# Optimization experiments

Hardware: AMD Instinct MI355X
Metric: run time of the kernel (lower is better)

## Reference

```python
import jax, jax.numpy as jnp
import numpy as np

B, NB, NS, C, HID, NP, NH = 8, 2048, 1024, 768, 3072, 1024, 6
HD = C // NH


def _ln(x, w, b):
    mu = x.mean(-1, keepdims=True)
    var = ((x - mu) ** 2).mean(-1, keepdims=True)
    return (x - mu) / jnp.sqrt(var + 1e-5) * w + b


def _gelu(z):
    return jax.nn.gelu(z, approximate=False)  # torch nn.GELU default = exact erf


def setup_inputs() -> dict:
    key = jax.random.key(0)
    ks = jax.random.split(key, 16)
    p = lambda i, shape: (jax.random.normal(ks[i], shape, jnp.float32) * 0.02)
    inp = {
        'x_b': jax.random.normal(ks[0], (B, NB, C), jnp.float32),
        'x_s': jax.random.normal(ks[1], (B, NS, C), jnp.float32),
        # token_types[0,0]=0 -> KV is computed (no stale cache), as on the first call
        'token_types': jax.random.randint(ks[2], (B, NS), 0, 2, jnp.int32).at[0, 0].set(0),
        'base_idxs': jax.random.randint(ks[3], (B, NP), -3, NB).astype(jnp.int32),
        'ln1_w': jnp.ones(C, jnp.float32), 'ln1_b': jnp.zeros(C, jnp.float32),
        'ln2_w': jnp.ones(C, jnp.float32), 'ln2_b': jnp.zeros(C, jnp.float32),
        'ln3_w': jnp.ones(C, jnp.float32), 'ln3_b': jnp.zeros(C, jnp.float32),
        'Wq': p(4, (C, C)), 'Wkv': p(5, (C, 2 * C)),
        'es_w1': p(6, (C, HID)), 'es_b1': jnp.zeros(HID, jnp.float32),
        'es_w2': p(7, (HID, C)), 'es_b2': jnp.zeros(C, jnp.float32),
        'el_w1': p(8, (C, HID)), 'el_b1': jnp.zeros(HID, jnp.float32),
        'el_w2': p(9, (HID, C)), 'el_b2': jnp.zeros(C, jnp.float32),
        'mlp_w1': p(10, (C, 4 * C)), 'mlp_b1': jnp.zeros(4 * C, jnp.float32),
        'mlp_w2': p(11, (4 * C, C)), 'mlp_b2': jnp.zeros(C, jnp.float32),
    }
    return inp


def reference(x_b, x_s, token_types, base_idxs,
              ln1_w, ln1_b, ln2_w, ln2_b, ln3_w, ln3_b,
              Wq, Wkv, es_w1, es_b1, es_w2, es_b2,
              el_w1, el_b1, el_w2, el_b2,
              mlp_w1, mlp_b1, mlp_w2, mlp_b2):
    Bn, Ns, Cd = x_s.shape
    # --- norm1/norm2 + cross-attention (q from x_s, kv from x_b) ---
    xs_n = _ln(x_s, ln1_w, ln1_b)
    xb_n = _ln(x_b, ln2_w, ln2_b)
    q = (xs_n @ Wq).reshape(Bn, Ns, NH, HD).transpose(0, 2, 1, 3)          # (B,H,Ns,hd)
    kv = (xb_n @ Wkv).reshape(Bn, -1, 2, NH, HD).transpose(2, 0, 3, 1, 4)  # (2,B,H,Nb,hd)
    k_, v_ = kv[0], kv[1]
    attn = jax.nn.softmax(jnp.einsum('bhqd,bhkd->bhqk', q, k_) * (HD ** -0.5), axis=-1)
    ctx = jnp.einsum('bhqk,bhkd->bhqd', attn, v_).transpose(0, 2, 1, 3).reshape(Bn, Ns, Cd)
    # --- 2-expert MoE MLP routed by token_types (0 -> expert_s, 1 -> expert_l) ---
    out_s = _gelu(ctx @ es_w1 + es_b1) @ es_w2 + es_b2
    out_l = _gelu(ctx @ el_w1 + el_b1) @ el_w2 + el_b2
    tt = token_types[..., None]
    moe = jnp.where(tt == 0, out_s, 0.0) + jnp.where(tt == 1, out_l, 0.0)
    x = x_s + moe
    # --- residual MLP ---
    x = x + (_gelu(_ln(x, ln3_w, ln3_b) @ mlp_w1 + mlp_b1) @ mlp_w2 + mlp_b2)
    x_norm = x / jnp.maximum(jnp.linalg.norm(x, axis=-1, keepdims=True), 1e-12)
    # --- masked-token kernel (vectorized over batch, masking replaces gather) ---
    nh = base_idxs.shape[1] // 2
    ids = base_idxs[:, :nh]
    mask = ids >= 0                                        # (B,nh)
    idc = jnp.where(mask, ids, 0)
    tokens = jnp.take_along_axis(x_b, idc[:, :, None], axis=1) * mask[..., None]
    sc = jnp.einsum('bic,bjc->bij', tokens, tokens) / jnp.sqrt(jnp.float32(Cd))
    kbias = jnp.where(mask, 0.0, -1e9)[:, None, :]
    aw = jax.nn.softmax(sc + kbias, axis=-1)
    agg = jnp.einsum('bij,bjc->bic', aw, tokens)
    cnt = mask.sum(-1)
    ksum = (agg * mask[..., None]).sum(1) / jnp.maximum(cnt, 1)[:, None]
    kn = ksum / jnp.maximum(jnp.linalg.norm(ksum, axis=-1, keepdims=True), 1e-12)
    has = (cnt > 0)[:, None]
    kernel = jnp.where(has, kn, 0.0)                        # (B,C)
    pos = jnp.where(has, (jnp.einsum('bnc,bc->bn', x_norm, kernel) + 1.0) / 2.0, 0.0)
    # --- top-k selection with data-dependent valid_k and straight-through binarize ---
    kk = Ns // 8
    topv, topi = jax.lax.top_k(pos, kk)
    cnt65 = (pos > 0.65).sum(-1)
    vk = jnp.minimum(kk, jnp.maximum(kk - 10, cnt65))
    keep = jnp.arange(kk)[None, :] < vk[:, None]
    vals = topv * keep
    sel = vals[:, :, None] * jax.nn.one_hot(topi, Ns, dtype=x.dtype)
    binary = (sel > 0.0).astype(x.dtype)
    sel = sel + jax.lax.stop_gradient(binary - sel)
    return sel, topi, pos, x, kernel[:, None, :]
```

## Files before the change

### kernel.cpp

```cpp
#include <hip/hip_runtime.h>
#include <hip/hip_bf16.h>
#include <math.h>

#define B_   8
#define NB_  2048
#define NS_  1024
#define Cc_  768
#define HID_ 3072
#define NP_  1024
#define NH_  6
#define HD_  128

__device__ __forceinline__ float gelu_exact(float v) {
  return 0.5f * v * (1.0f + erff(v * 0.7071067811865476f));
}

__device__ __forceinline__ void split3(float v, unsigned short& h,
                                       unsigned short& m, unsigned short& l) {
  unsigned hb = __float_as_uint(v) & 0xffff0000u;
  float r1 = v - __uint_as_float(hb);
  unsigned mb = __float_as_uint(r1) & 0xffff0000u;
  float r2 = r1 - __uint_as_float(mb);
  unsigned lb = __float_as_uint(r2) & 0xffff0000u;
  h = (unsigned short)(hb >> 16);
  m = (unsigned short)(mb >> 16);
  l = (unsigned short)(lb >> 16);
}

typedef short bf16x8 __attribute__((ext_vector_type(8)));
typedef float f32x4 __attribute__((ext_vector_type(4)));

#define BLOCK_REDUCE_ADD(red, tid)                                              \
  for (int off_ = 128; off_; off_ >>= 1) {                                      \
    if ((tid) < off_) red[(tid)] += red[(tid) + off_];                          \
    __syncthreads();                                                            \
  }

__global__ __launch_bounds__(256) void ln_split(
    const float* __restrict__ x, unsigned short* __restrict__ y,
    const float* __restrict__ w, const float* __restrict__ b) {
  __shared__ float red[256];
  int row = blockIdx.x, tid = threadIdx.x;
  const float* xr = x + (size_t)row * Cc_;
  float v0 = xr[tid], v1 = xr[tid + 256], v2 = xr[tid + 512];
  red[tid] = v0 + v1 + v2;
  __syncthreads();
  BLOCK_REDUCE_ADD(red, tid);
  float mu = red[0] / (float)Cc_;
  __syncthreads();
  float d0 = v0 - mu, d1 = v1 - mu, d2 = v2 - mu;
  red[tid] = d0 * d0 + d1 * d1 + d2 * d2;
  __syncthreads();
  BLOCK_REDUCE_ADD(red, tid);
  float var = red[0] / (float)Cc_;
  float rs = 1.0f / sqrtf(var + 1e-5f);
  unsigned short* yr = y + (size_t)row * 2304;
  float vals[3] = {d0 * rs * w[tid] + b[tid],
                   d1 * rs * w[tid + 256] + b[tid + 256],
                   d2 * rs * w[tid + 512] + b[tid + 512]};
#pragma unroll
  for (int t = 0; t < 3; ++t) {
    int c = tid + (t << 8);
    unsigned short h16, m16, l16;
    split3(vals[t], h16, m16, l16);
    yr[c] = h16; yr[768 + c] = m16; yr[1536 + c] = l16;
  }
}

__global__ __launch_bounds__(256) void split_kernel(
    const float* __restrict__ x, unsigned short* __restrict__ y) {
  size_t idx = (size_t)blockIdx.x * 256 + threadIdx.x;
  int c = (int)(idx % Cc_);
  int row = (int)(idx / Cc_);
  unsigned short h16, m16, l16;
  split3(x[idx], h16, m16, l16);
  unsigned short* yr = y + (size_t)row * 2304;
  yr[c] = h16; yr[768 + c] = m16; yr[1536 + c] = l16;
}

__global__ __launch_bounds__(256) void qsplit(
    const float* __restrict__ q, unsigned short* __restrict__ qp) {
  int idx = blockIdx.x * 256 + threadIdx.x;
  int c = idx & 127, m = (idx >> 7) & 1023, h = idx >> 17;
  float v = q[(size_t)m * 768 + h * 128 + c];
  unsigned short h16, m16, l16;
  split3(v, h16, m16, l16);
  size_t base = (size_t)h * 393216 + (size_t)m * 384;
  qp[base + c] = h16; qp[base + 128 + c] = m16; qp[base + 256 + c] = l16;
}

__global__ __launch_bounds__(256) void ksplit(
    const float* __restrict__ kv, unsigned short* __restrict__ kp) {
  int idx = blockIdx.x * 256 + threadIdx.x;
  int c = idx & 127, n = (idx >> 7) & 2047, h = idx >> 18;
  float v = kv[(size_t)n * 1536 + h * 128 + c];
  unsigned short h16, m16, l16;
  split3(v, h16, m16, l16);
  size_t base = (size_t)h * 786432 + (size_t)n * 384;
  kp[base + c] = h16; kp[base + 128 + c] = m16; kp[base + 256 + c] = l16;
}

__global__ __launch_bounds__(256) void rownorm_kernel(
    const float* __restrict__ x, float* __restrict__ y) {
  __shared__ float red[256];
  int row = blockIdx.x, tid = threadIdx.x;
  const float* xr = x + (size_t)row * Cc_;
  float* yr = y + (size_t)row * Cc_;
  float v0 = xr[tid], v1 = xr[tid + 256], v2 = xr[tid + 512];
  red[tid] = v0 * v0 + v1 * v1 + v2 * v2;
  __syncthreads();
  BLOCK_REDUCE_ADD(red, tid);
  float den = fmaxf(sqrtf(red[0]), 1e-12f);
  yr[tid]       = v0 / den;
  yr[tid + 256] = v1 / den;
  yr[tid + 512] = v2 / den;
}

__global__ __launch_bounds__(256) void wconv(
    const float* __restrict__ W, unsigned short* __restrict__ out,
    int K, int N, int ldw, int ncol0) {
  int k = blockIdx.x * 256 + threadIdx.x;
  int n = blockIdx.y;
  float v = W[(size_t)k * ldw + ncol0 + n];
  unsigned short h16, m16, l16;
  split3(v, h16, m16, l16);
  size_t base = (size_t)n * 3 * K;
  out[base + k] = h16;
  out[base + K + k] = m16;
  out[base + 2 * K + k] = l16;
}

template <int EPI, bool AGATHER, bool MDEV>
__global__ __launch_bounds__(256) void mgemm(
    const unsigned short* __restrict__ Ap, const unsigned short* __restrict__ Bp,
    float* __restrict__ Cf, unsigned short* __restrict__ Cs,
    const float* __restrict__ bias,
    const int* __restrict__ perm, const int* __restrict__ mdev,
    int M, int N, int K, int ldc, int Kout, int nsplit,
    long azs, long bzs, long zstride, float scale) {
  __shared__ unsigned short As[2][8192];
  __shared__ unsigned short Bs[2][8192];
  int z = blockIdx.z;
  int gx = gridDim.x;
  int id = blockIdx.y * gx + blockIdx.x;
  int per = (gx * gridDim.y) >> 3;
  int nid = (id & 7) * per + (id >> 3);
  int bx = nid % gx, by = nid / gx;
  int Me = MDEV ? mdev[0] : M;
  int m0 = by * 128, n0 = bx * 128;
  if (MDEV && m0 >= Me) return;
  const unsigned short* ApB = Ap + (size_t)z * azs;
  const unsigned short* BpB = Bp + (size_t)z * bzs;
  int tid = threadIdx.x;
  int lane = tid & 63, w = tid >> 6;
  int wr = w >> 1, wc = w & 1;
  int K3 = 3 * K;
  int tps = K >> 6;
  int KT = 6 * tps;
  int span = KT / nsplit;
  int zr = z % nsplit;
  int tt0 = zr * span, tt1 = tt0 + span;

  const unsigned short* agp[4];
  const unsigned short* bgp[4];
  int wswz[4];
#pragma unroll
  for (int p = 0; p < 4; ++p) {
    int r = (tid >> 3) + 32 * p;
    int ma = m0 + r;
    if (MDEV) ma = min(ma, Me - 1);
    if (AGATHER) ma = perm[ma];
    agp[p] = ApB + (size_t)ma * K3 + (tid & 7) * 8;
    bgp[p] = BpB + (size_t)(n0 + r) * K3 + (tid & 7) * 8;
    wswz[p] = r * 64 + (((tid & 7) ^ (r & 7)) << 3);
  }

  f32x4 acc[4][4];
  f32x4 zero4 = {0.f, 0.f, 0.f, 0.f};
#pragma unroll
  for (int i = 0; i < 4; ++i)
#pragma unroll
    for (int j = 0; j < 4; ++j) acc[i][j] = zero4;

  int kg = lane >> 4;
  int frm[4], frn[4];
#pragma unroll
  for (int f = 0; f < 4; ++f) {
    frm[f] = wr * 64 + f * 16 + (lane & 15);
    frn[f] = wc * 64 + f * 16 + (lane & 15);
  }

  bf16x8 ra[4], rb[4];
  {
    int seg = tt0 / tps, kt = tt0 - seg * tps;
    int pa = (0x210100u >> (4 * seg)) & 0xF;
    int pb = (0x012010u >> (4 * seg)) & 0xF;
    size_t ao = (size_t)(pa * K + kt * 64);
    size_t bo = (size_t)(pb * K + kt * 64);
#pragma unroll
    for (int p = 0; p < 4; ++p) {
      ra[p] = *(const bf16x8*)(agp[p] + ao);
      rb[p] = *(const bf16x8*)(bgp[p] + bo);
    }
  }

  for (int tt = tt0; tt < tt1; ++tt) {
    int cur = tt & 1;
#pragma unroll
    for (int p = 0; p < 4; ++p) {
      *(bf16x8*)&As[cur][wswz[p]] = ra[p];
      *(bf16x8*)&Bs[cur][wswz[p]] = rb[p];
    }
    if (tt + 1 < tt1) {
      int seg = (tt + 1) / tps, kt = (tt + 1) - seg * tps;
      int pa = (0x210100u >> (4 * seg)) & 0xF;
      int pb = (0x012010u >> (4 * seg)) & 0xF;
      size_t ao = (size_t)(pa * K + kt * 64);
      size_t bo = (size_t)(pb * K + kt * 64);
#pragma unroll
      for (int p = 0; p < 4; ++p) {
        ra[p] = *(const bf16x8*)(agp[p] + ao);
        rb[p] = *(const bf16x8*)(bgp[p] + bo);
      }
    }
    asm volatile("s_waitcnt lgkmcnt(0)" ::: "memory");
    __builtin_amdgcn_s_barrier();
#pragma unroll
    for (int ks = 0; ks < 2; ++ks) {
      int ch = ks * 4 + kg;
      bf16x8 af[4], bf[4];
#pragma unroll
      for (int f = 0; f < 4; ++f) {
        int r = frm[f];
        af[f] = *(const bf16x8*)&As[cur][r * 64 + ((ch ^ (r & 7)) << 3)];
      }
#pragma unroll
      for (int f = 0; f < 4; ++f) {
        int r = frn[f];
        bf[f] = *(const bf16x8*)&Bs[cur][r * 64 + ((ch ^ (r & 7)) << 3)];
      }
#pragma unroll
      for (int i = 0; i < 4; ++i)
#pragma unroll
        for (int j = 0; j < 4; ++j)
          acc[i][j] = __builtin_amdgcn_mfma_f32_16x16x32_bf16(
              af[i], bf[j], acc[i][j], 0, 0, 0);
    }
  }

#pragma unroll
  for (int i = 0; i < 4; ++i) {
#pragma unroll
    for (int r = 0; r < 4; ++r) {
      int m = m0 + wr * 64 + i * 16 + kg * 4 + r;
      if (MDEV && m >= Me) continue;
#pragma unroll
      for (int j = 0; j < 4; ++j) {
        int n = n0 + wc * 64 + j * 16 + (lane & 15);
        float v = acc[i][j][r] * scale;
        if (EPI == 6) {
          Cf[(size_t)z * zstride + (size_t)m * ldc + n] = v;
        } else if (EPI == 7) {
          Cf[(size_t)z * zstride + (size_t)m * ldc + n] += v;
        } else if (EPI == 5) {
          float t = gelu_exact(v + bias[n]);
          unsigned short h16, m16, l16;
          split3(t, h16, m16, l16);
          size_t base = (size_t)m * 3 * Kout;
          Cs[base + n] = h16;
          Cs[base + Kout + n] = m16;
          Cs[base + 2 * Kout + n] = l16;
        }
      }
    }
  }
}

template <bool SCATTER>
__global__ __launch_bounds__(256) void combineP(
    const float* __restrict__ P0, const float* __restrict__ P1,
    const float* __restrict__ bias, const float* __restrict__ addsrc,
    const int* __restrict__ perm, const int* __restrict__ cnt,
    float* __restrict__ out) {
  int m = blockIdx.x;
  int c = threadIdx.x + (blockIdx.y << 8);
  if (SCATTER && m >= cnt[0]) return;
  int mo = SCATTER ? perm[m] : m;
  size_t pm = (size_t)m * 768 + c;
  out[(size_t)mo * 768 + c] =
      bias[c] + addsrc[(size_t)mo * 768 + c] + P0[pm] + P1[pm];
}

template <int EPI, int TRB, bool AGATHER, bool MDEV>
__global__ __launch_bounds__(256) void gemm128(
    const float* __restrict__ A, const float* __restrict__ Bm,
    float* __restrict__ Cm, const float* __restrict__ bias,
    const float* __restrict__ addsrc, const int* __restrict__ perm,
    const int* __restrict__ mdev,
    int M, int N, int K, int lda, int ldb, int ldc,
    int d1, int d2,
    long a_s1, long a_s2, long a_s3,
    long b_s1, long b_s2, long b_s3,
    long c_s1, long c_s2, long c_s3,
    float scale) {
  __shared__ float As[2][16][132];
  __shared__ float Bs[2][16][132];
  int z = blockIdx.z;
  int z1 = z / (d1 * d2);
  int rem = z - z1 * d1 * d2;
  int z2 = rem / d2, z3 = rem - z2 * d2;
  const float* Ab = A + (size_t)z1 * a_s1 + (size_t)z2 * a_s2 + (size_t)z3 * a_s3;
  const float* Bb = Bm + (size_t)z1 * b_s1 + (size_t)z2 * b_s2 + (size_t)z3 * b_s3;
  float* Cb = Cm + (size_t)z1 * c_s1 + (size_t)z2 * c_s2 + (size_t)z3 * c_s3;
  int Me = MDEV ? mdev[0] : M;
  int m0 = blockIdx.y * 128, n0 = blockIdx.x * 128;
  if (MDEV && m0 >= Me) return;
  int tid = threadIdx.x;
  int tx = tid & 15, ty = tid >> 4;
  int arow = tid >> 2, akq = tid & 3;
  int ma0 = m0 + arow, ma1 = m0 + arow + 64;
  if (MDEV) { ma0 = min(ma0, Me - 1); ma1 = min(ma1, Me - 1); }
  if (AGATHER) { ma0 = perm[ma0]; ma1 = perm[ma1]; }
  const float* Ap0 = Ab + (size_t)ma0 * lda + akq * 4;
  const float* Ap1 = Ab + (size_t)ma1 * lda + akq * 4;
  const float* Bp0;
  const float* Bp1;
  int bw_r0 = 0, bw_c0 = 0, bw_r1 = 0;
  if (TRB == 0) {
    bw_r0 = tid >> 5; bw_c0 = (tid & 31) * 4; bw_r1 = bw_r0 + 8;
    Bp0 = Bb + (size_t)bw_r0 * ldb + n0 + bw_c0;
    Bp1 = Bb + (size_t)bw_r1 * ldb + n0 + bw_c0;
  } else {
    Bp0 = Bb + (size_t)(n0 + arow) * ldb + akq * 4;
    Bp1 = Bb + (size_t)(n0 + arow + 64) * ldb + akq * 4;
  }
  float4 pa0 = *(const float4*)Ap0;
  float4 pa1 = *(const float4*)Ap1;
  float4 pb0 = *(const float4*)Bp0;
  float4 pb1 = *(const float4*)Bp1;
  float acc[8][8] = {};
  int nt = K >> 4;
  for (int t = 0; t < nt; ++t) {
    int cur = t & 1;
    As[cur][akq * 4 + 0][arow] = pa0.x; As[cur][akq * 4 + 1][arow] = pa0.y;
    As[cur][akq * 4 + 2][arow] = pa0.z; As[cur][akq * 4 + 3][arow] = pa0.w;
    As[cur][akq * 4 + 0][arow + 64] = pa1.x; As[cur][akq * 4 + 1][arow + 64] = pa1.y;
    As[cur][akq * 4 + 2][arow + 64] = pa1.z; As[cur][akq * 4 + 3][arow + 64] = pa1.w;
    if (TRB == 0) {
      *(float4*)&Bs[cur][bw_r0][bw_c0] = pb0;
      *(float4*)&Bs[cur][bw_r1][bw_c0] = pb1;
    } else {
      Bs[cur][akq * 4 + 0][arow] = pb0.x; Bs[cur][akq * 4 + 1][arow] = pb0.y;
      Bs[cur][akq * 4 + 2][arow] = pb0.z; Bs[cur][akq * 4 + 3][arow] = pb0.w;
      Bs[cur][akq * 4 + 0][arow + 64] = pb1.x; Bs[cur][akq * 4 + 1][arow + 64] = pb1.y;
      Bs[cur][akq * 4 + 2][arow + 64] = pb1.z; Bs[cur][akq * 4 + 3][arow + 64] = pb1.w;
    }
    if (t + 1 < nt) {
      int kn = (t + 1) << 4;
      pa0 = *(const float4*)&Ap0[kn];
      pa1 = *(const float4*)&Ap1[kn];
      if (TRB == 0) {
        pb0 = *(const float4*)&Bp0[(size_t)kn * ldb];
        pb1 = *(const float4*)&Bp1[(size_t)kn * ldb];
      } else {
        pb0 = *(const float4*)&Bp0[kn];
        pb1 = *(const float4*)&Bp1[kn];
      }
    }
    asm volatile("s_waitcnt lgkmcnt(0)" ::: "memory");
    __builtin_amdgcn_s_barrier();
#pragma unroll
    for (int kk = 0; kk < 16; ++kk) {
      float a[8], b[8];
      *(float4*)&a[0] = *(const float4*)&As[cur][kk][ty * 4];
      *(float4*)&a[4] = *(const float4*)&As[cur][kk][ty * 4 + 64];
      *(float4*)&b[0] = *(const float4*)&Bs[cur][kk][tx * 4];
      *(float4*)&b[4] = *(const float4*)&Bs[cur][kk][tx * 4 + 64];
#pragma unroll
      for (int i = 0; i < 8; ++i)
#pragma unroll
        for (int j = 0; j < 8; ++j)
          acc[i][j] = fmaf(a[i], b[j], acc[i][j]);
    }
  }
#pragma unroll
  for (int i = 0; i < 8; ++i) {
    int m = m0 + ((i < 4) ? (ty * 4 + i) : (64 + ty * 4 + i - 4));
    if (!MDEV || m < Me) {
      int mo = (EPI == 4) ? perm[m] : m;
      int n = n0 + tx * 4;
      float v[8];
#pragma unroll
      for (int j = 0; j < 8; ++j) {
        int nj = (j < 4) ? (n + j) : (n + 64 + j - 4);
        v[j] = acc[i][j] * scale;
        if (EPI >= 1) v[j] += bias[nj];
        if (EPI == 2) v[j] = gelu_exact(v[j]);
        if (EPI == 3 || EPI == 4) v[j] += addsrc[(size_t)mo * ldc + nj];
      }
      float* cp = &Cb[(size_t)mo * ldc + n];
      *(float4*)cp = make_float4(v[0], v[1], v[2], v[3]);
      *(float4*)(cp + 64) = make_float4(v[4], v[5], v[6], v[7]);
    }
  }
}

__global__ __launch_bounds__(256) void pv_reduce(
    const float* __restrict__ part, float* __restrict__ ctx) {
  int i = blockIdx.x * 256 + threadIdx.x;
  int n = i & 127, m = (i >> 7) & 1023, h = i >> 17;
  float s = 0.f;
#pragma unroll
  for (int ks = 0; ks < 8; ++ks)
    s += part[(size_t)(ks * 6 + h) * 131072 + m * 128 + n];
  ctx[(size_t)m * 768 + h * 128 + n] = s;
}

template <int EPT, bool MASK>
__global__ __launch_bounds__(256) void softmax_kernel(
    float* __restrict__ s, const float* __restrict__ maskf) {
  __shared__ float red[256];
  int row = blockIdx.x, tid = threadIdx.x;
  float* sr = s + (size_t)row * (EPT * 256);
  const float* mb = MASK ? (maskf + (size_t)(row / 512) * 512) : nullptr;
  float v[EPT];
  float m = -3.0e38f;
#pragma unroll
  for (int t = 0; t < EPT; ++t) {
    int j = tid + (t << 8);
    float xv = sr[j];
    if (MASK) xv += (mb[j] != 0.0f) ? 0.0f : -1e9f;
    v[t] = xv;
    m = fmaxf(m, xv);
  }
  red[tid] = m;
  __syncthreads();
  for (int off = 128; off; off >>= 1) {
    if (tid < off) red[tid] = fmaxf(red[tid], red[tid + off]);
    __syncthreads();
  }
  m = red[0];
  __syncthreads();
  float ssum = 0.f;
#pragma unroll
  for (int t = 0; t < EPT; ++t) {
    v[t] = expf(v[t] - m);
    ssum += v[t];
  }
  red[tid] = ssum;
  __syncthreads();
  BLOCK_REDUCE_ADD(red, tid);
  float tot = red[0];
#pragma unroll
  for (int t = 0; t < EPT; ++t) sr[tid + (t << 8)] = v[t] / tot;
}

__global__ __launch_bounds__(256) void build_perm(
    const int* __restrict__ tt, int* __restrict__ perm0,
    int* __restrict__ perm1, int* __restrict__ cnt) {
  int r = blockIdx.x * 256 + threadIdx.x;
  int t = tt[r];
  if (t == 0) { int p = atomicAdd(&cnt[0], 1); perm0[p] = r; }
  else        { int p = atomicAdd(&cnt[1], 1); perm1[p] = r; }
}

__global__ __launch_bounds__(256) void gather_kernel(
    const float* __restrict__ xb, const int* __restrict__ bidx,
    float* __restrict__ tokens, float* __restrict__ maskf) {
  size_t idx = (size_t)blockIdx.x * 256 + threadIdx.x;
  int c = (int)(idx % Cc_);
  int i = (int)((idx / Cc_) % 512);
  int b = (int)(idx / ((size_t)Cc_ * 512));
  int id = bidx[b * NP_ + i];
  bool m = id >= 0;
  int idc = m ? id : 0;
  tokens[idx] = m ? xb[((size_t)b * NB_ + idc) * Cc_ + c] : 0.0f;
  if (c == 0) maskf[b * 512 + i] = m ? 1.0f : 0.0f;
}

__global__ __launch_bounds__(256) void kernel_kernel(
    const float* __restrict__ agg, const float* __restrict__ maskf,
    float* __restrict__ kern, float* __restrict__ hasf) {
  __shared__ float red[256];
  __shared__ float ks[Cc_];
  __shared__ float s_cnt;
  int b = blockIdx.x, tid = threadIdx.x;
  const float* mb = maskf + b * 512;
  red[tid] = mb[tid] + mb[tid + 256];
  __syncthreads();
  BLOCK_REDUCE_ADD(red, tid);
  if (tid == 0) s_cnt = red[0];
  __syncthreads();
  float cnt = s_cnt;
  float dc = fmaxf(cnt, 1.0f);
  const float* ab = agg + (size_t)b * 512 * Cc_;
#pragma unroll
  for (int t = 0; t < 3; ++t) {
    int cc = tid + t * 256;
    float s = 0.f;
    for (int i = 0; i < 512; ++i) s = fmaf(ab[(size_t)i * Cc_ + cc], mb[i], s);
    ks[cc] = s / dc;
  }
  __syncthreads();
  float s2 = 0.f;
#pragma unroll
  for (int t = 0; t < 3; ++t) {
    float q = ks[tid + t * 256];
    s2 = fmaf(q, q, s2);
  }
  red[tid] = s2;
  __syncthreads();
  BLOCK_REDUCE_ADD(red, tid);
  float den = fmaxf(sqrtf(red[0]), 1e-12f);
  bool has = cnt > 0.5f;
#pragma unroll
  for (int t = 0; t < 3; ++t) {
    int cc = tid + t * 256;
    kern[(size_t)b * Cc_ + cc] = has ? (ks[cc] / den) : 0.0f;
  }
  if (tid == 0) hasf[b] = has ? 1.0f : 0.0f;
}

__global__ __launch_bounds__(256) void pos_kernel(
    const float* __restrict__ xnorm, const float* __restrict__ kern,
    const float* __restrict__ hasf, float* __restrict__ pos) {
  __shared__ float red[256];
  int row = blockIdx.x, tid = threadIdx.x;
  int b = row >> 10;
  const float* xr = xnorm + (size_t)row * Cc_;
  const float* kr = kern + (size_t)b * Cc_;
  float s = xr[tid] * kr[tid];
  s = fmaf(xr[tid + 256], kr[tid + 256], s);
  s = fmaf(xr[tid + 512], kr[tid + 512], s);
  red[tid] = s;
  __syncthreads();
  BLOCK_REDUCE_ADD(red, tid);
  if (tid == 0) pos[row] = (hasf[b] > 0.5f) ? (red[0] + 1.0f) * 0.5f : 0.0f;
}

__global__ __launch_bounds__(256) void topk_kernel(
    const float* __restrict__ pos, float* __restrict__ sel,
    float* __restrict__ topi) {
  __shared__ float vals[NS_];
  __shared__ float rv[256];
  __shared__ int ri[256];
  __shared__ int s_vk;
  int b = blockIdx.x, tid = threadIdx.x;
  const float* pr = pos + (size_t)b * NS_;
  int c65 = 0;
#pragma unroll
  for (int t = 0; t < 4; ++t) {
    float v = pr[tid + (t << 8)];
    vals[tid + (t << 8)] = v;
    if (v > 0.65f) ++c65;
  }
  ri[tid] = c65;
  __syncthreads();
  for (int off = 128; off; off >>= 1) {
    if (tid < off) ri[tid] += ri[tid + off];
    __syncthreads();
  }
  if (tid == 0) {
    int vk = ri[0] > 118 ? ri[0] : 118;
    s_vk = vk > 128 ? 128 : vk;
  }
  __syncthreads();
  int vk = s_vk;
  for (int r = 0; r < 128; ++r) {
    float bv = -3.0e38f;
    int bi = 0x7fffffff;
#pragma unroll
    for (int t = 0; t < 4; ++t) {
      int i = tid + (t << 8);
      float v = vals[i];
      if (v > bv) { bv = v; bi = i; }
    }
    rv[tid] = bv; ri[tid] = bi;
    __syncthreads();
    for (int off = 128; off; off >>= 1) {
      if (tid < off) {
        float ov = rv[tid + off]; int oi = ri[tid + off];
        if (ov > rv[tid] || (ov == rv[tid] && oi < ri[tid])) {
          rv[tid] = ov; ri[tid] = oi;
        }
      }
      __syncthreads();
    }
    if (tid == 0) {
      int wi = ri[0]; float wv = rv[0];
      topi[(size_t)b * 128 + r] = (float)wi;
      if (r < vk && wv > 0.0f) sel[((size_t)b * 128 + r) * NS_ + wi] = 1.0f;
      vals[wi] = -3.0e38f;
    }
    __syncthreads();
  }
}

extern "C" void kernel_launch(void* const* d_in, const int* in_sizes, int n_in,
                              void* d_out, int out_size, void* d_ws, size_t ws_size,
                              hipStream_t stream) {
  (void)in_sizes; (void)n_in; (void)out_size; (void)ws_size;
  const float* x_b = (const float*)d_in[0];
  const float* x_s = (const float*)d_in[1];
  const int* token_types = (const int*)d_in[2];
  const int* base_idxs = (const int*)d_in[3];
  const float* ln1_w = (const float*)d_in[4];
  const float* ln1_b = (const float*)d_in[5];
  const float* ln2_w = (const float*)d_in[6];
  const float* ln2_b = (const float*)d_in[7];
  const float* ln3_w = (const float*)d_in[8];
  const float* ln3_b = (const float*)d_in[9];
  const float* Wq = (const float*)d_in[10];
  const float* Wkv = (const float*)d_in[11];
  const float* es_w1 = (const float*)d_in[12];
  const float* es_b1 = (const float*)d_in[13];
  const float* es_w2 = (const float*)d_in[14];
  const float* es_b2 = (const float*)d_in[15];
  const float* el_w1 = (const float*)d_in[16];
  const float* el_b1 = (const float*)d_in[17];
  const float* el_w2 = (const float*)d_in[18];
  const float* el_b2 = (const float*)d_in[19];
  const float* mlp_w1 = (const float*)d_in[20];
  const float* mlp_b1 = (const float*)d_in[21];
  const float* mlp_w2 = (const float*)d_in[22];
  const float* mlp_b2 = (const float*)d_in[23];

  float* out = (float*)d_out;
  float* sel_out  = out;
  float* topi_out = out + 1048576;
  float* pos_out  = out + 1049600;
  float* x_out    = out + 1057792;
  float* kern_out = out + 7349248;

  float* w = (float*)d_ws;
  float* kv_f = w;
  float* q_f  = w + 25165824;
  float* scores = w + 31457280;
  float* part   = w + 44040192;
  float* ctxf   = w + 50331648;
  unsigned short* qp_b = (unsigned short*)(w + 56623104);
  unsigned short* kp_b = (unsigned short*)(w + 57802752);
  unsigned short* xbnp = (unsigned short*)(w + 31457280);
  unsigned short* xsnp = (unsigned short*)(w + 50331648);
  unsigned short* wqp  = (unsigned short*)(w + 59768832);
  unsigned short* wkvp = (unsigned short*)(w + 60653568);
  unsigned short* ctxp = (unsigned short*)(w + 6291456);
  unsigned short* wb   = (unsigned short*)(w + 15728640);
  unsigned short* hp   = (unsigned short*)(w + 36962304);
  float* P0 = w;
  const long ZS = 55836672;
  float* P1 = w + ZS;
  float* xn     = w + 6291456;
  float* tokens = w + 12582912;
  float* aw     = w + 15728640;
  float* agg    = w + 17825792;
  float* small  = w + 62914560;
  float* maskf  = small;
  float* hasf   = small + 4096;
  int* cnt      = (int*)(small + 4104);
  int* perm0    = (int*)(small + 4106);
  int* perm1    = (int*)(small + 12298);

  unsigned short* esw1h[2] = {wb + 0,        wb + 3538944};
  unsigned short* elw1h[2] = {wb + 7077888,  wb + 10616832};
  unsigned short* mlw1h[2] = {wb + 14155776, wb + 17694720};
  unsigned short* esw2h[2] = {wb + 21233664, wb + 24772608};
  unsigned short* elw2h[2] = {wb + 28311552, wb + 31850496};
  unsigned short* mlw2h[2] = {wb + 35389440, wb + 38928384};

  const long NSC = (long)NS_ * Cc_;
  const long NB2C = (long)NB_ * 2 * Cc_;
  const long SNB = (long)NS_ * NB_;
  const float qk_scale = 0.08838834764831845f;
  const float sc_scale = 0.036084391824351615f;

  hipMemsetAsync(sel_out, 0, (size_t)1048576 * sizeof(float), stream);
  hipMemsetAsync(cnt, 0, 2 * sizeof(int), stream);

  ln_split<<<B_ * NS_, 256, 0, stream>>>(x_s, xsnp, ln1_w, ln1_b);
  ln_split<<<B_ * NB_, 256, 0, stream>>>(x_b, xbnp, ln2_w, ln2_b);
  build_perm<<<32, 256, 0, stream>>>(token_types, perm0, perm1, cnt);
  wconv<<<dim3(3, 768), 256, 0, stream>>>(Wq, wqp, 768, 768, 768, 0);
  wconv<<<dim3(3, 1536), 256, 0, stream>>>(Wkv, wkvp, 768, 1536, 1536, 0);
  mgemm<6, false, false><<<dim3(6, 64, 1), 256, 0, stream>>>(
      xsnp, wqp, q_f, nullptr, nullptr, nullptr, nullptr,
      8192, 768, 768, 768, 0, 1, 0, 0, 0, 1.0f);
  mgemm<6, false, false><<<dim3(12, 128, 1), 256, 0, stream>>>(
      xbnp, wkvp, kv_f, nullptr, nullptr, nullptr, nullptr,
      16384, 1536, 768, 1536, 0, 1, 0, 0, 0, 1.0f);

  for (int b = 0; b < B_; ++b) {
    const float* qb = q_f + (size_t)b * NSC;
    const float* kvb = kv_f + (size_t)b * NB2C;
    const float* vb = kvb + Cc_;
    qsplit<<<3072, 256, 0, stream>>>(qb, qp_b);
    ksplit<<<6144, 256, 0, stream>>>(kvb, kp_b);
    mgemm<6, false, false><<<dim3(16, 8, 6), 256, 0, stream>>>(
        qp_b, kp_b, scores, nullptr, nullptr, nullptr, nullptr,
        1024, 2048, 128, 2048, 0, 1, 393216, 786432, SNB, qk_scale);
    softmax_kernel<8, false><<<6 * 1024, 256, 0, stream>>>(scores, nullptr);
    gemm128<0, 0, false, false><<<dim3(1, 8, 48), 256, 0, stream>>>(
        scores, vb, part, nullptr, nullptr, nullptr, nullptr,
        1024, 128, 256, 2048, 1536, 128,
        6, 8, 0, SNB, 256, 0, 128, 393216, 0, 131072, 786432, 1.0f);
    pv_reduce<<<3072, 256, 0, stream>>>(part, ctxf + (size_t)b * NSC);
  }

  split_kernel<<<24576, 256, 0, stream>>>(ctxf, ctxp);
  for (int h = 0; h < 2; ++h) {
    wconv<<<dim3(3, 1536), 256, 0, stream>>>(es_w1, esw1h[h], 768, 1536, 3072, h * 1536);
    wconv<<<dim3(3, 1536), 256, 0, stream>>>(el_w1, elw1h[h], 768, 1536, 3072, h * 1536);
    wconv<<<dim3(3, 1536), 256, 0, stream>>>(mlp_w1, mlw1h[h], 768, 1536, 3072, h * 1536);
    wconv<<<dim3(6, 768), 256, 0, stream>>>(es_w2 + (size_t)h * 1536 * 768, esw2h[h], 1536, 768, 768, 0);
    wconv<<<dim3(6, 768), 256, 0, stream>>>(el_w2 + (size_t)h * 1536 * 768, elw2h[h], 1536, 768, 768, 0);
    wconv<<<dim3(6, 768), 256, 0, stream>>>(mlp_w2 + (size_t)h * 1536 * 768, mlw2h[h], 1536, 768, 768, 0);
  }

  for (int h = 0; h < 2; ++h) {
    mgemm<5, true, true><<<dim3(12, 64, 1), 256, 0, stream>>>(
        ctxp, esw1h[h], nullptr, hp, es_b1 + h * 1536, perm0, cnt,
        8192, 1536, 768, 0, 1536, 1, 0, 0, 0, 1.0f);
    if (h == 0)
      mgemm<6, false, true><<<dim3(6, 64, 2), 256, 0, stream>>>(
          hp, esw2h[h], P0, nullptr, nullptr, nullptr, cnt,
          8192, 768, 1536, 768, 0, 2, 0, 0, ZS, 1.0f);
    else
      mgemm<7, false, true><<<dim3(6, 64, 2), 256, 0, stream>>>(
          hp, esw2h[h], P0, nullptr, nullptr, nullptr, cnt,
          8192, 768, 1536, 768, 0, 2, 0, 0, ZS, 1.0f);
  }
  combineP<true><<<dim3(8192, 3), 256, 0, stream>>>(
      P0, P1, es_b2, x_s, perm0, cnt, x_out);
  for (int h = 0; h < 2; ++h) {
    mgemm<5, true, true><<<dim3(12, 64, 1), 256, 0, stream>>>(
        ctxp, elw1h[h], nullptr, hp, el_b1 + h * 1536, perm1, cnt + 1,
        8192, 1536, 768, 0, 1536, 1, 0, 0, 0, 1.0f);
    if (h == 0)
      mgemm<6, false, true><<<dim3(6, 64, 2), 256, 0, stream>>>(
          hp, elw2h[h], P0, nullptr, nullptr, nullptr, cnt + 1,
          8192, 768, 1536, 768, 0, 2, 0, 0, ZS, 1.0f);
    else
      mgemm<7, false, true><<<dim3(6, 64, 2), 256, 0, stream>>>(
          hp, elw2h[h], P0, nullptr, nullptr, nullptr, cnt + 1,
          8192, 768, 1536, 768, 0, 2, 0, 0, ZS, 1.0f);
  }
  combineP<true><<<dim3(8192, 3), 256, 0, stream>>>(
      P0, P1, el_b2, x_s, perm1, cnt + 1, x_out);
  ln_split<<<B_ * NS_, 256, 0, stream>>>(x_out, ctxp, ln3_w, ln3_b);
  for (int h = 0; h < 2; ++h) {
    mgemm<5, false, false><<<dim3(12, 64, 1), 256, 0, stream>>>(
        ctxp, mlw1h[h], nullptr, hp, mlp_b1 + h * 1536, nullptr, nullptr,
        8192, 1536, 768, 0, 1536, 1, 0, 0, 0, 1.0f);
    if (h == 0)
      mgemm<6, false, false><<<dim3(6, 64, 2), 256, 0, stream>>>(
          hp, mlw2h[h], P0, nullptr, nullptr, nullptr, nullptr,
          8192, 768, 1536, 768, 0, 2, 0, 0, ZS, 1.0f);
    else
      mgemm<7, false, false><<<dim3(6, 64, 2), 256, 0, stream>>>(
          hp, mlw2h[h], P0, nullptr, nullptr, nullptr, nullptr,
          8192, 768, 1536, 768, 0, 2, 0, 0, ZS, 1.0f);
  }
  combineP<false><<<dim3(8192, 3), 256, 0, stream>>>(
      P0, P1, mlp_b2, x_out, nullptr, nullptr, x_out);

  rownorm_kernel<<<B_ * NS_, 256, 0, stream>>>(x_out, xn);
  gather_kernel<<<12288, 256, 0, stream>>>(x_b, base_idxs, tokens, maskf);
  gemm128<0, 1, false, false><<<dim3(4, 4, 8), 256, 0, stream>>>(
      tokens, tokens, aw, nullptr, nullptr, nullptr, nullptr,
      512, 512, 768, 768, 768, 512,
      1, 1, 393216, 0, 0, 393216, 0, 0, 262144, 0, 0, sc_scale);
  softmax_kernel<2, true><<<8 * 512, 256, 0, stream>>>(aw, maskf);
  gemm128<0, 0, false, false><<<dim3(6, 4, 8), 256, 0, stream>>>(
      aw, tokens, agg, nullptr, nullptr, nullptr, nullptr,
      512, 768, 512, 512, 768, 768,
      1, 1, 262144, 0, 0, 393216, 0, 0, 393216, 0, 0, 1.0f);
  kernel_kernel<<<8, 256, 0, stream>>>(agg, maskf, kern_out, hasf);
  pos_kernel<<<B_ * NS_, 256, 0, stream>>>(xn, kern_out, hasf, pos_out);
  topk_kernel<<<8, 256, 0, stream>>>(pos_out, sel_out, topi_out);
}
```

Measured before the change: 3.725 ms.

## Compute QK^T with fp32 gemm128 directly and split PV over more K chunks

Removes the per-batch qsplit/ksplit kernels and the 3-way bf16-split mgemm for attention scores. QK^T now runs through the existing fp32 gemm128 kernel, reading Q and K in place with strided layouts. The PV product is split into 16 K-chunks of 128 instead of 8 of 256, which doubles the grid, and pv_reduce sums 16 partials. Softmax also switches to the fast __expf. These remove the split passes and add parallelism, at the cost of possibly slower fp32 FMA versus matrix-core bf16x3, and slightly lower exp accuracy.

```diff
diff --git a/kernel.cpp b/kernel.cpp
--- a/kernel.cpp
+++ b/kernel.cpp
@@ -76,28 +76,6 @@
   split3(x[idx], h16, m16, l16);
   unsigned short* yr = y + (size_t)row * 2304;
   yr[c] = h16; yr[768 + c] = m16; yr[1536 + c] = l16;
-}
-
-__global__ __launch_bounds__(256) void qsplit(
-    const float* __restrict__ q, unsigned short* __restrict__ qp) {
-  int idx = blockIdx.x * 256 + threadIdx.x;
-  int c = idx & 127, m = (idx >> 7) & 1023, h = idx >> 17;
-  float v = q[(size_t)m * 768 + h * 128 + c];
-  unsigned short h16, m16, l16;
-  split3(v, h16, m16, l16);
-  size_t base = (size_t)h * 393216 + (size_t)m * 384;
-  qp[base + c] = h16; qp[base + 128 + c] = m16; qp[base + 256 + c] = l16;
-}
-
-__global__ __launch_bounds__(256) void ksplit(
-    const float* __restrict__ kv, unsigned short* __restrict__ kp) {
-  int idx = blockIdx.x * 256 + threadIdx.x;
-  int c = idx & 127, n = (idx >> 7) & 2047, h = idx >> 18;
-  float v = kv[(size_t)n * 1536 + h * 128 + c];
-  unsigned short h16, m16, l16;
-  split3(v, h16, m16, l16);
-  size_t base = (size_t)h * 786432 + (size_t)n * 384;
-  kp[base + c] = h16; kp[base + 128 + c] = m16; kp[base + 256 + c] = l16;
 }
 
 __global__ __launch_bounds__(256) void rownorm_kernel(
@@ -411,7 +389,7 @@
   int n = i & 127, m = (i >> 7) & 1023, h = i >> 17;
   float s = 0.f;
 #pragma unroll
-  for (int ks = 0; ks < 8; ++ks)
+  for (int ks = 0; ks < 16; ++ks)
     s += part[(size_t)(ks * 6 + h) * 131072 + m * 128 + n];
   ctx[(size_t)m * 768 + h * 128 + n] = s;
 }
@@ -444,7 +422,7 @@
   float ssum = 0.f;
 #pragma unroll
   for (int t = 0; t < EPT; ++t) {
-    v[t] = expf(v[t] - m);
+    v[t] = __expf(v[t] - m);
     ssum += v[t];
   }
   red[tid] = ssum;
@@ -637,9 +615,7 @@
   float* q_f  = w + 25165824;
   float* scores = w + 31457280;
   float* part   = w + 44040192;
-  float* ctxf   = w + 50331648;
-  unsigned short* qp_b = (unsigned short*)(w + 56623104);
-  unsigned short* kp_b = (unsigned short*)(w + 57802752);
+  float* ctxf   = w + 56623104;
   unsigned short* xbnp = (unsigned short*)(w + 31457280);
   unsigned short* xsnp = (unsigned short*)(w + 50331648);
   unsigned short* wqp  = (unsigned short*)(w + 59768832);
@@ -691,18 +667,17 @@
 
   for (int b = 0; b < B_; ++b) {
     const float* qb = q_f + (size_t)b * NSC;
-    const float* kvb = kv_f + (size_t)b * NB2C;
-    const float* vb = kvb + Cc_;
-    qsplit<<<3072, 256, 0, stream>>>(qb, qp_b);
-    ksplit<<<6144, 256, 0, stream>>>(kvb, kp_b);
-    mgemm<6, false, false><<<dim3(16, 8, 6), 256, 0, stream>>>(
-        qp_b, kp_b, scores, nullptr, nullptr, nullptr, nullptr,
-        1024, 2048, 128, 2048, 0, 1, 393216, 786432, SNB, qk_scale);
+    const float* kb = kv_f + (size_t)b * NB2C;
+    const float* vb = kb + Cc_;
+    gemm128<0, 1, false, false><<<dim3(16, 8, 6), 256, 0, stream>>>(
+        qb, kb, scores, nullptr, nullptr, nullptr, nullptr,
+        1024, 2048, 128, 768, 1536, 2048,
+        1, 1, 128, 0, 0, 128, 0, 0, SNB, 0, 0, qk_scale);
     softmax_kernel<8, false><<<6 * 1024, 256, 0, stream>>>(scores, nullptr);
-    gemm128<0, 0, false, false><<<dim3(1, 8, 48), 256, 0, stream>>>(
+    gemm128<0, 0, false, false><<<dim3(1, 8, 96), 256, 0, stream>>>(
         scores, vb, part, nullptr, nullptr, nullptr, nullptr,
-        1024, 128, 256, 2048, 1536, 128,
-        6, 8, 0, SNB, 256, 0, 128, 393216, 0, 131072, 786432, 1.0f);
+        1024, 128, 128, 2048, 1536, 128,
+        6, 16, 0, SNB, 128, 0, 128, 128 * 1536, 0, 131072, 786432, 1.0f);
     pv_reduce<<<3072, 256, 0, stream>>>(part, ctxf + (size_t)b * NSC);
   }
 
```

Result: slower. 3.801 ms (+2.0%).
